# Optimization experiments

Measured on AMD Instinct MI355X. Metric: run time of the kernel, lower is better.

Reference implementation:

```python
import jax, jax.numpy as jnp
import numpy as np
from jax import lax

B, C, H, W = 8, 128, 128, 128
KS = 5  # Pascal/binomial kernel size


def _pascal_kernel_2d(ks: int) -> np.ndarray:
    # Row `ks` of Pascal's triangle, e.g. ks=5 -> [1,4,6,4,1]
    row = np.array([1.0])
    for _ in range(ks - 1):
        row = np.convolve(row, [1.0, 1.0])
    k2d = np.outer(row, row)
    return (k2d / k2d.sum()).astype(np.float32)


def setup_inputs() -> dict:
    key = jax.random.key(0)
    x = jax.random.normal(key, (B, C, H, W), dtype=jnp.float32)
    k2d = _pascal_kernel_2d(KS)  # (5,5), normalized binomial
    # Depthwise conv weight: (out_ch=C, in_ch/groups=1, KS, KS)
    kernel = jnp.broadcast_to(jnp.asarray(k2d)[None, None], (C, 1, KS, KS))
    return {"x": x, "kernel": kernel, "scale_factor": 2}


def reference(x, kernel, scale_factor):
    s = scale_factor
    b, c, h, w = x.shape
    # strided_upsampling2d: inject zeros as rows/cols
    up = jnp.zeros((b, c, h * s, w * s), dtype=x.dtype)
    up = up.at[:, :, ::s, ::s].set(x)
    # PascalFilter2d: depthwise conv, padding = KS//2 (same spatial size)
    pad = KS // 2
    out = lax.conv_general_dilated(
        up, kernel,
        window_strides=(1, 1),
        padding=[(pad, pad), (pad, pad)],
        dimension_numbers=("NCHW", "OIHW", "NCHW"),
        feature_group_count=c,
    )
    return out
```

## Files before the change

kernel.cpp:

```cpp
#include <hip/hip_runtime.h>


#define BB 8
#define CC 128
#define HH 128
#define WW 128

typedef float f32x2 __attribute__((ext_vector_type(2)));
typedef float f32x4 __attribute__((ext_vector_type(4)));

__global__ __launch_bounds__(256) void upfilter2d_kernel(
    const float* __restrict__ x,
    float* __restrict__ out)
{
    int tid  = blockIdx.x * blockDim.x + threadIdx.x;
    int lane = tid & 63;
    int w    = tid >> 6;
    int y    = w & (HH - 1);
    int bc   = w >> 7;

    const float* xp = x + (size_t)bc * (HH * WW) + 2 * lane;

    f32x2 v0, v1, v2;
    {
        f32x2 z = {0.f, 0.f};
        v0 = (y > 0)      ? *reinterpret_cast<const f32x2*>(xp + (y - 1) * WW) : z;
        v1 =                *reinterpret_cast<const f32x2*>(xp + y * WW);
        v2 = (y < HH - 1) ? *reinterpret_cast<const f32x2*>(xp + (y + 1) * WW) : z;
    }

    float tE0 = (v0.x + v2.x) + 6.f * v1.x;
    float tE1 = (v0.y + v2.y) + 6.f * v1.y;
    float tO0 = v1.x + v2.x;
    float tO1 = v1.y + v2.y;

    float tEm = __shfl_up(tE1, 1);   if (lane == 0)  tEm = 0.f;
    float tOm = __shfl_up(tO1, 1);   if (lane == 0)  tOm = 0.f;
    float tEp = __shfl_down(tE0, 1); if (lane == 63) tEp = 0.f;
    float tOp = __shfl_down(tO0, 1); if (lane == 63) tOp = 0.f;

    f32x4 oE, oO;
    oE.x = ((tEm + tE1) + 6.f * tE0) * 0.00390625f;
    oE.y = (tE0 + tE1) * 0.015625f;
    oE.z = ((tE0 + tEp) + 6.f * tE1) * 0.00390625f;
    oE.w = (tE1 + tEp) * 0.015625f;
    oO.x = ((tOm + tO1) + 6.f * tO0) * 0.015625f;
    oO.y = (tO0 + tO1) * 0.0625f;
    oO.z = ((tO0 + tOp) + 6.f * tO1) * 0.015625f;
    oO.w = (tO1 + tOp) * 0.0625f;

    const int OW = 2 * WW;
    float* op = out + (size_t)bc * (2 * HH * OW) + (size_t)(2 * y) * OW + 4 * lane;
    *reinterpret_cast<f32x4*>(op)      = oE;
    *reinterpret_cast<f32x4*>(op + OW) = oO;
}

extern "C" void kernel_launch(void* const* d_in, const int* in_sizes, int n_in,
                              void* d_out, int out_size, void* d_ws, size_t ws_size,
                              hipStream_t stream) {
    const float* x = (const float*)d_in[0];
    float* out = (float*)d_out;

    int nblk = BB * CC * HH / 4;
    dim3 grid(nblk), block(256);

    upfilter2d_kernel<<<grid, block, 0, stream>>>(x, out);
}
```

Measured before the change: 71.39 us.

## Process four output row pairs per wave and swizzle block order

Each wavefront now handles four input rows and loads six input rows, where before every row needed three loads. This cuts redundant global reads from 3x to 1.5x per row and quarters the grid size. The block index is also swizzled in strided groups of eight, which changes which blocks run concurrently and may affect L2/channel locality. The cost is fewer waves in flight and more registers per thread.

```diff
diff --git a/kernel.cpp b/kernel.cpp
--- a/kernel.cpp
+++ b/kernel.cpp
@@ -5,6 +5,7 @@
 #define CC 128
 #define HH 128
 #define WW 128
+#define RR 4
 
 typedef float f32x2 __attribute__((ext_vector_type(2)));
 typedef float f32x4 __attribute__((ext_vector_type(4)));
@@ -13,46 +14,55 @@
     const float* __restrict__ x,
     float* __restrict__ out)
 {
-    int tid  = blockIdx.x * blockDim.x + threadIdx.x;
+    int bid = blockIdx.x;
+    int swz = (bid & 7) * ((BB * CC * (HH / RR) * 64 / 256) >> 3) + (bid >> 3);
+    int tid = swz * 256 + (int)threadIdx.x;
+
     int lane = tid & 63;
     int w    = tid >> 6;
-    int y    = w & (HH - 1);
-    int bc   = w >> 7;
+    int rg   = w & (HH / RR - 1);
+    int bc   = w >> 5;
+    int y0   = rg * RR;
 
     const float* xp = x + (size_t)bc * (HH * WW) + 2 * lane;
 
-    f32x2 v0, v1, v2;
-    {
-        f32x2 z = {0.f, 0.f};
-        v0 = (y > 0)      ? *reinterpret_cast<const f32x2*>(xp + (y - 1) * WW) : z;
-        v1 =                *reinterpret_cast<const f32x2*>(xp + y * WW);
-        v2 = (y < HH - 1) ? *reinterpret_cast<const f32x2*>(xp + (y + 1) * WW) : z;
-    }
-
-    float tE0 = (v0.x + v2.x) + 6.f * v1.x;
-    float tE1 = (v0.y + v2.y) + 6.f * v1.y;
-    float tO0 = v1.x + v2.x;
-    float tO1 = v1.y + v2.y;
-
-    float tEm = __shfl_up(tE1, 1);   if (lane == 0)  tEm = 0.f;
-    float tOm = __shfl_up(tO1, 1);   if (lane == 0)  tOm = 0.f;
-    float tEp = __shfl_down(tE0, 1); if (lane == 63) tEp = 0.f;
-    float tOp = __shfl_down(tO0, 1); if (lane == 63) tOp = 0.f;
-
-    f32x4 oE, oO;
-    oE.x = ((tEm + tE1) + 6.f * tE0) * 0.00390625f;
-    oE.y = (tE0 + tE1) * 0.015625f;
-    oE.z = ((tE0 + tEp) + 6.f * tE1) * 0.00390625f;
-    oE.w = (tE1 + tEp) * 0.015625f;
-    oO.x = ((tOm + tO1) + 6.f * tO0) * 0.015625f;
-    oO.y = (tO0 + tO1) * 0.0625f;
-    oO.z = ((tO0 + tOp) + 6.f * tO1) * 0.015625f;
-    oO.w = (tO1 + tOp) * 0.0625f;
+    f32x2 v[RR + 2];
+    f32x2 z = {0.f, 0.f};
+    v[0] = (rg > 0) ? *reinterpret_cast<const f32x2*>(xp + (y0 - 1) * WW) : z;
+#pragma unroll
+    for (int r = 1; r <= RR; ++r)
+        v[r] = *reinterpret_cast<const f32x2*>(xp + (y0 + r - 1) * WW);
+    v[RR + 1] = (rg < HH / RR - 1)
+        ? *reinterpret_cast<const f32x2*>(xp + (y0 + RR) * WW) : z;
 
     const int OW = 2 * WW;
-    float* op = out + (size_t)bc * (2 * HH * OW) + (size_t)(2 * y) * OW + 4 * lane;
-    *reinterpret_cast<f32x4*>(op)      = oE;
-    *reinterpret_cast<f32x4*>(op + OW) = oO;
+    float* op = out + (size_t)bc * (2 * HH * OW) + (size_t)(2 * y0) * OW + 4 * lane;
+
+#pragma unroll
+    for (int r = 0; r < RR; ++r) {
+        float tE0 = (v[r].x + v[r + 2].x) + 6.f * v[r + 1].x;
+        float tE1 = (v[r].y + v[r + 2].y) + 6.f * v[r + 1].y;
+        float tO0 = v[r + 1].x + v[r + 2].x;
+        float tO1 = v[r + 1].y + v[r + 2].y;
+
+        float tEm = __shfl_up(tE1, 1);   if (lane == 0)  tEm = 0.f;
+        float tOm = __shfl_up(tO1, 1);   if (lane == 0)  tOm = 0.f;
+        float tEp = __shfl_down(tE0, 1); if (lane == 63) tEp = 0.f;
+        float tOp = __shfl_down(tO0, 1); if (lane == 63) tOp = 0.f;
+
+        f32x4 oE, oO;
+        oE.x = ((tEm + tE1) + 6.f * tE0) * 0.00390625f;
+        oE.y = (tE0 + tE1) * 0.015625f;
+        oE.z = ((tE0 + tEp) + 6.f * tE1) * 0.00390625f;
+        oE.w = (tE1 + tEp) * 0.015625f;
+        oO.x = ((tOm + tO1) + 6.f * tO0) * 0.015625f;
+        oO.y = (tO0 + tO1) * 0.0625f;
+        oO.z = ((tO0 + tOp) + 6.f * tO1) * 0.015625f;
+        oO.w = (tO1 + tOp) * 0.0625f;
+
+        *reinterpret_cast<f32x4*>(op + (2 * r) * OW)     = oE;
+        *reinterpret_cast<f32x4*>(op + (2 * r + 1) * OW) = oO;
+    }
 }
 
 extern "C" void kernel_launch(void* const* d_in, const int* in_sizes, int n_in,
@@ -61,8 +71,6 @@
     const float* x = (const float*)d_in[0];
     float* out = (float*)d_out;
 
-    int nblk = BB * CC * HH / 4;
-    dim3 grid(nblk), block(256);
-
-    upfilter2d_kernel<<<grid, block, 0, stream>>>(x, out);
+    int nblk = BB * CC * (HH / RR) * 64 / 256;
+    upfilter2d_kernel<<<dim3(nblk), dim3(256), 0, stream>>>(x, out);
 }
```

Measured after the change: 83.39 us. 1.17x slower.
